# Kernel optimization log

Hardware: AMD Instinct MI355X
Metric: run time of the kernel (lower is better)

Reference implementation:

```python
import jax, jax.numpy as jnp
import numpy as np

NUM_HEADS = 16
EMBED_DIM = 1024
HEAD_DIM = EMBED_DIM // NUM_HEADS
REG_LEN = 2048
SUM_LEN = 64
BSZ = 2
REL_DIM = 64
NUM_REL_EMB = 64
MAX_SUMMARY = 64
SCALE = HEAD_DIM ** -0.5


def _ln(x, g, b, eps=1e-5):
    m = jnp.mean(x, axis=-1, keepdims=True)
    v = jnp.mean((x - m) ** 2, axis=-1, keepdims=True)
    return (x - m) * jax.lax.rsqrt(v + eps) * g + b


def setup_inputs() -> dict:
    key = jax.random.key(0)
    ks = jax.random.split(key, 16)
    inp = {}
    inp['reg_x'] = jax.random.normal(ks[0], (REG_LEN, BSZ, EMBED_DIM), jnp.float32)
    inp['sum_token_ids'] = jax.random.randint(ks[1], (BSZ, SUM_LEN), 0, MAX_SUMMARY + 1)
    inp['rel_idx'] = jax.random.randint(ks[2], (BSZ, SUM_LEN + REG_LEN, REG_LEN), 0, NUM_REL_EMB)
    inp['sum_len'] = SUM_LEN
    inp['reg_len'] = REG_LEN
    emb = jax.random.normal(ks[3], (MAX_SUMMARY + 1, EMBED_DIM), jnp.float32) * 0.02
    inp['emb_sum'] = emb.at[0].set(0.0)  # padding_idx = 0
    inp['rel_emb0'] = jax.random.normal(ks[4], (NUM_REL_EMB, REL_DIM), jnp.float32) * 0.02

    def lin(k, din, dout):
        return jax.random.normal(k, (din, dout), jnp.float32) * (1.0 / np.sqrt(din))

    inp['Wq'] = lin(ks[5], EMBED_DIM, EMBED_DIM); inp['bq'] = jnp.zeros((EMBED_DIM,), jnp.float32)
    inp['Wk'] = lin(ks[6], EMBED_DIM, EMBED_DIM); inp['bk'] = jnp.zeros((EMBED_DIM,), jnp.float32)
    inp['Wv'] = lin(ks[7], EMBED_DIM, EMBED_DIM); inp['bv'] = jnp.zeros((EMBED_DIM,), jnp.float32)
    inp['Wr0'] = lin(ks[8], REL_DIM, EMBED_DIM); inp['br0'] = jnp.zeros((EMBED_DIM,), jnp.float32)
    inp['Wk2'] = lin(ks[9], HEAD_DIM, HEAD_DIM); inp['bk2'] = jnp.zeros((HEAD_DIM,), jnp.float32)
    inp['Wv2'] = lin(ks[10], HEAD_DIM, HEAD_DIM); inp['bv2'] = jnp.zeros((HEAD_DIM,), jnp.float32)
    inp['Wo'] = lin(ks[11], EMBED_DIM, EMBED_DIM); inp['bo'] = jnp.zeros((EMBED_DIM,), jnp.float32)
    for name in ['ln_k', 'ln_v', 'ln_k2', 'ln_v2']:
        inp[name + '_g'] = jnp.ones((HEAD_DIM,), jnp.float32)
        inp[name + '_b'] = jnp.zeros((HEAD_DIM,), jnp.float32)
    return inp


def reference(reg_x, sum_token_ids, rel_idx, sum_len, reg_len, emb_sum, rel_emb0,
              Wq, bq, Wk, bk, Wv, bv, Wr0, br0, Wk2, bk2, Wv2, bv2, Wo, bo,
              ln_k_g, ln_k_b, ln_v_g, ln_v_b, ln_k2_g, ln_k2_b, ln_v2_g, ln_v2_b):
    R, B, E = reg_x.shape  # reg_len, bsz, embed_dim
    H, D = NUM_HEADS, HEAD_DIM
    S = sum_token_ids.shape[1]

    # regular K/V projections + per-head LayerNorm
    reg_k = _ln((reg_x @ Wk + bk).reshape(R, B, H, D), ln_k_g, ln_k_b)
    reg_v = _ln((reg_x @ Wv + bv).reshape(R, B, H, D), ln_v_g, ln_v_b)

    # relation-type embedding projection -> [Rrel, H, D]
    r0 = (rel_emb0 @ Wr0 + br0).reshape(NUM_REL_EMB, H, D)

    # --- stage 1: summary tokens attend over regular tokens ---
    sum_x = emb_sum[sum_token_ids.T]                     # [S, B, E]
    sum_q = sum_x.reshape(S, B, H, D) * SCALE
    scores_sum = jnp.einsum('sbhd,kbhd->bhsk', sum_q, reg_k)   # [B,H,S,R]
    qr_sum = jnp.einsum('sbhd,Zhd->bhsZ', sum_q, r0)           # [B,H,S,Rrel]
    idx_sum = rel_idx[:, :S]                                   # [B,S,R]
    scores_sum = scores_sum + jnp.take_along_axis(qr_sum, idx_sum[:, None, :, :], axis=-1)
    w_sum = jax.nn.softmax(scores_sum, axis=-1)
    sum_x2 = jnp.einsum('bhsk,kbhd->sbhd', w_sum, reg_v)       # [S,B,H,D]

    sum_k2 = _ln(sum_x2 @ Wk2 + bk2, ln_k2_g, ln_k2_b)
    sum_v2 = _ln(sum_x2 @ Wv2 + bv2, ln_v2_g, ln_v2_b)

    # --- stage 2: regular tokens attend over [summary ; regular] keys ---
    reg_q = (reg_x @ Wq + bq).reshape(R, B, H, D) * SCALE
    scores_rs = jnp.einsum('qbhd,sbhd->bhqs', reg_q, sum_k2)   # [B,H,R,S]
    scores_rr = jnp.einsum('qbhd,kbhd->bhqk', reg_q, reg_k)    # [B,H,R,R]
    qr_reg = jnp.einsum('qbhd,Zhd->bhqZ', reg_q, r0)
    idx_reg = rel_idx[:, S:]                                   # [B,R,R]
    scores_rr = scores_rr + jnp.take_along_axis(qr_reg, idx_reg[:, None, :, :], axis=-1)
    scores = jnp.concatenate([scores_rs, scores_rr], axis=-1)  # [B,H,R,S+R]
    w = jax.nn.softmax(scores, axis=-1)
    v_all = jnp.concatenate([sum_v2, reg_v], axis=0)           # [S+R,B,H,D]
    attn_out = jnp.einsum('bhqk,kbhd->qbhd', w, v_all).reshape(R, B, E)
    reg_x2 = attn_out @ Wo + bo
    return reg_x2
```

## Files before the change

### kernel.cpp

```cpp
#include <hip/hip_runtime.h>
#include <cstdint>
#include <cstddef>

#define NH   16
#define HD   64
#define RLEN 2048
#define BSZ  2
#define SLEN 64
#define NZ   64
#define ED   1024
#define KTOT 2112
#define NSPLIT 16

#define QSCALE 0.18033688011112042f

typedef __bf16 bf16_t;
typedef bf16_t bf16x8 __attribute__((ext_vector_type(8)));
typedef bf16_t bf16x4 __attribute__((ext_vector_type(4)));
typedef float  f32x4  __attribute__((ext_vector_type(4)));

__device__ __forceinline__ f32x4 mfma16(bf16x8 a, bf16x8 b, f32x4 c) {
    return __builtin_amdgcn_mfma_f32_16x16x32_bf16(a, b, c, 0, 0, 0);
}

__device__ __forceinline__ void dma16(const void* g, void* l) {
    __builtin_amdgcn_global_load_lds(
        (const __attribute__((address_space(1))) unsigned int*)g,
        (__attribute__((address_space(3))) unsigned int*)l, 16, 0, 0);
}


template<int BM>
__global__ __launch_bounds__(256) void gemm_fast(
    const bf16_t* __restrict__ A, const bf16_t* __restrict__ Bt,
    const float* __restrict__ b0, const float* __restrict__ b1,
    const float* __restrict__ b2,
    const float* __restrict__ gk_, const float* __restrict__ bk_,
    const float* __restrict__ gv_, const float* __restrict__ bv_,
    bf16_t* __restrict__ oq, float* __restrict__ o1,
    bf16_t* __restrict__ okf, bf16_t* __restrict__ ovf,
    int M, int K, int N, int mode)
{
    constexpr int MT = BM / 64;
    __shared__ __align__(16) bf16_t As[BM * 64];
    __shared__ __align__(16) bf16_t Bs[128 * 64];
    __shared__ __align__(16) bf16_t trs[64][66];

    const int t = threadIdx.x;
    const int wave = t >> 6, lane = t & 63;
    const int quad = lane >> 4, l15 = lane & 15;
    const int rsub = lane >> 3, gq = lane & 7;
    const int m0 = blockIdx.y * BM, n0 = blockIdx.x * 128;

    f32x4 acc[MT][8];
#pragma unroll
    for (int i = 0; i < MT; i++)
#pragma unroll
        for (int j = 0; j < 8; j++) acc[i][j] = (f32x4){0.f, 0.f, 0.f, 0.f};

    for (int k0 = 0; k0 < K; k0 += 64) {
#pragma unroll
        for (int j = 0; j < BM / 32; j++) {
            int row = wave * (BM / 4) + j * 8 + rsub;
            const bf16_t* g = A + (size_t)(m0 + row) * K + k0 + ((gq ^ (row & 7)) * 8);
            dma16(g, As + (wave * (BM / 4) + j * 8) * 64);
        }
#pragma unroll
        for (int j = 0; j < 4; j++) {
            int row = wave * 32 + j * 8 + rsub;
            const bf16_t* g = Bt + (size_t)(n0 + row) * K + k0 + ((gq ^ (row & 7)) * 8);
            dma16(g, Bs + (wave * 32 + j * 8) * 64);
        }
        __syncthreads();

#pragma unroll
        for (int kk = 0; kk < 2; kk++) {
            const int pg = ((kk * 4 + quad) ^ (l15 & 7)) * 8;
            bf16x8 af[MT], bf[8];
#pragma unroll
            for (int mt = 0; mt < MT; mt++)
                af[mt] = *(const bf16x8*)(As + (wave * (BM / 4) + mt * 16 + l15) * 64 + pg);
#pragma unroll
            for (int nt = 0; nt < 8; nt++)
                bf[nt] = *(const bf16x8*)(Bs + (nt * 16 + l15) * 64 + pg);
#pragma unroll
            for (int mt = 0; mt < MT; mt++)
#pragma unroll
                for (int nt = 0; nt < 8; nt++)
                    acc[mt][nt] = mfma16(af[mt], bf[nt], acc[mt][nt]);
        }
        __syncthreads();
    }

    if (mode == 0) {
#pragma unroll
        for (int mt = 0; mt < MT; mt++)
#pragma unroll
            for (int nt = 0; nt < 8; nt++)
#pragma unroll
                for (int reg = 0; reg < 4; reg++) {
                    int m = m0 + wave * (BM / 4) + mt * 16 + quad * 4 + reg;
                    int n = n0 + nt * 16 + l15;
                    o1[(size_t)m * N + n] = acc[mt][nt][reg] + b0[n];
                }
        return;
    }

    const int seg = n0 >> 10;
    if (seg == 0) {
#pragma unroll
        for (int mt = 0; mt < MT; mt++)
#pragma unroll
            for (int nt = 0; nt < 8; nt++)
#pragma unroll
                for (int reg = 0; reg < 4; reg++) {
                    int m = m0 + wave * (BM / 4) + mt * 16 + quad * 4 + reg;
                    int n = n0 + nt * 16 + l15;
                    float c = acc[mt][nt][reg] + b0[n];
                    int h = n >> 6, d = n & 63;
                    int r = m >> 1, bb2 = m & 1;
                    size_t off = (((size_t)bb2 * NH + h) * RLEN + r) * HD + d;
                    oq[off] = (bf16_t)(c * QSCALE);
                }
        return;
    }

    const int nl0 = n0 & 1023, h0 = nl0 >> 6;
    const float* bias = (seg == 1) ? b1 : b2;
    const float* lg = (seg == 1) ? gk_ : gv_;
    const float* lb = (seg == 1) ? bk_ : bv_;
    float gj[4], bj[4], bsv[2][4];
#pragma unroll
    for (int j = 0; j < 4; j++) { gj[j] = lg[j * 16 + l15]; bj[j] = lb[j * 16 + l15]; }
#pragma unroll
    for (int h2 = 0; h2 < 2; h2++)
#pragma unroll
        for (int j = 0; j < 4; j++)
            bsv[h2][j] = bias[nl0 + (h2 * 4 + j) * 16 + l15];

    if (seg == 1) {
#pragma unroll
        for (int mt = 0; mt < MT; mt++)
#pragma unroll
            for (int reg = 0; reg < 4; reg++) {
                int m = m0 + wave * (BM / 4) + mt * 16 + quad * 4 + reg;
                int r = m >> 1, bb2 = m & 1, rt = r & 63;
#pragma unroll
                for (int h2 = 0; h2 < 2; h2++) {
                    float c[4], s1 = 0.f, s2 = 0.f;
#pragma unroll
                    for (int j = 0; j < 4; j++) {
                        c[j] = acc[mt][h2 * 4 + j][reg] + bsv[h2][j];
                        s1 += c[j]; s2 += c[j] * c[j];
                    }
#pragma unroll
                    for (int o = 1; o < 16; o <<= 1) {
                        s1 += __shfl_xor(s1, o);
                        s2 += __shfl_xor(s2, o);
                    }
                    float mean = s1 * (1.f / 64.f);
                    float rsi = rsqrtf(s2 * (1.f / 64.f) - mean * mean + 1e-5f);
                    size_t base = (size_t)(bb2 * NH + h0 + h2) * 131072
                                + (size_t)(r >> 6) * 4096;
#pragma unroll
                    for (int j = 0; j < 4; j++) {
                        int d = j * 16 + l15;
                        float y = (c[j] - mean) * rsi * gj[j] + bj[j];
                        okf[base + (size_t)((((rt & 3) * 2 + (d >> 5)) * 64
                              + ((d >> 3) & 3) * 16 + (rt >> 2)) * 8 + (d & 7))] = (bf16_t)y;
                    }
                }
            }
    } else {
        const int tidx = m0 >> 7;
        const int dd = t >> 2, rs2 = (t & 3) * 16;
#pragma unroll
        for (int pb = 0; pb < 2; pb++)
#pragma unroll
            for (int h2 = 0; h2 < 2; h2++) {
#pragma unroll
                for (int mt = 0; mt < MT; mt++)
#pragma unroll
                    for (int rsel = 0; rsel < 2; rsel++) {
                        const int reg = pb + 2 * rsel;
                        const int key = wave * (BM / 8) + mt * 8 + quad * 2 + rsel;
                        float c[4], s1 = 0.f, s2 = 0.f;
#pragma unroll
                        for (int j = 0; j < 4; j++) {
                            c[j] = acc[mt][h2 * 4 + j][reg] + bsv[h2][j];
                            s1 += c[j]; s2 += c[j] * c[j];
                        }
#pragma unroll
                        for (int o = 1; o < 16; o <<= 1) {
                            s1 += __shfl_xor(s1, o);
                            s2 += __shfl_xor(s2, o);
                        }
                        float mean = s1 * (1.f / 64.f);
                        float rsi = rsqrtf(s2 * (1.f / 64.f) - mean * mean + 1e-5f);
#pragma unroll
                        for (int j = 0; j < 4; j++) {
                            float y = (c[j] - mean) * rsi * gj[j] + bj[j];
                            trs[key][j * 16 + l15] = (bf16_t)y;
                        }
                    }
                __syncthreads();
                {
                    bf16x8 o0v, o1v;
#pragma unroll
                    for (int j = 0; j < 8; j++) {
                        o0v[j] = trs[rs2 + j][dd];
                        o1v[j] = trs[rs2 + 8 + j][dd];
                    }
                    size_t base = (size_t)(pb * NH + h0 + h2) * 131072;
                    size_t off0 = base + (size_t)((((tidx * 4 + (dd >> 4)) * 2 + (rs2 >> 5)) * 64
                                  + ((rs2 >> 3) & 3) * 16 + (dd & 15)) * 8);
                    int rsb = rs2 + 8;
                    size_t off1 = base + (size_t)((((tidx * 4 + (dd >> 4)) * 2 + (rsb >> 5)) * 64
                                  + ((rsb >> 3) & 3) * 16 + (dd & 15)) * 8);
                    *(bf16x8*)(ovf + off0) = o0v;
                    *(bf16x8*)(ovf + off1) = o1v;
                }
                __syncthreads();
            }
    }
}

__global__ __launch_bounds__(256) void prep_batch(
    const float* __restrict__ regx, bf16_t* __restrict__ xb,
    const float* __restrict__ Wq, const float* __restrict__ Wk,
    const float* __restrict__ Wv, const float* __restrict__ Wo,
    bf16_t* __restrict__ wqt, bf16_t* __restrict__ wkt,
    bf16_t* __restrict__ wvt, bf16_t* __restrict__ wot,
    const float* __restrict__ emb, const int* __restrict__ ids,
    bf16_t* __restrict__ sum_q,
    const float* __restrict__ rel_emb0, const float* __restrict__ Wr0,
    const float* __restrict__ br0, float* __restrict__ r0out)
{
    const int t = threadIdx.x;
    if (blockIdx.x < 4096) {
        int i = (blockIdx.x * 256 + t) * 4;
        float4 v = *(const float4*)(regx + i);
        bf16x4 o;
        o[0] = (bf16_t)v.x; o[1] = (bf16_t)v.y; o[2] = (bf16_t)v.z; o[3] = (bf16_t)v.w;
        *(bf16x4*)(xb + i) = o;
        return;
    }
    const int bid = blockIdx.x - 4096;

    if (bid >= 1152) {
        const int h = bid - 1152;
        __shared__ float relT[64][65];
        __shared__ float Wl[64][64];
#pragma unroll
        for (int i = 0; i < 4; i++) {
            int idx = t + i * 256;
            int rr = idx >> 4, c4 = (idx & 15) * 4;
            float4 rv = *(const float4*)(rel_emb0 + rr * 64 + c4);
            relT[c4][rr] = rv.x; relT[c4 + 1][rr] = rv.y;
            relT[c4 + 2][rr] = rv.z; relT[c4 + 3][rr] = rv.w;
            float4 wv = *(const float4*)(Wr0 + (size_t)rr * ED + h * 64 + c4);
            *(float4*)(&Wl[rr][c4]) = wv;
        }
        __syncthreads();
        const int z = t & 63, dq = t >> 6;
        float a2[16];
#pragma unroll
        for (int i = 0; i < 16; i++) a2[i] = br0[h * 64 + dq * 16 + i];
        for (int k = 0; k < 64; k++) {
            float r = relT[k][z];
#pragma unroll
            for (int i = 0; i < 16; i++) a2[i] += r * Wl[k][dq * 16 + i];
        }
        float* dst = r0out + ((size_t)h * NZ + z) * HD + dq * 16;
#pragma unroll
        for (int i = 0; i < 4; i++)
            *(float4*)(dst + i * 4) = *(float4*)(&a2[i * 4]);
        return;
    }
    if (bid >= 1024) {
        int sb = bid - 1024;
        int s = sb >> 1, b = sb & 1;
        int id = ids[b * SLEN + s];
        const float* src = emb + (size_t)id * ED;
        for (int e = t; e < ED; e += 256) {
            int h = e >> 6, d = e & 63;
            sum_q[(((size_t)b * NH + h) * SLEN + s) * HD + d] = (bf16_t)(src[e] * QSCALE);
        }
        return;
    }

    __shared__ float tile[64][65];
    int sel = bid >> 8, local = bid & 255;
    const float* src = (sel == 0) ? Wq : (sel == 1) ? Wk : (sel == 2) ? Wv : Wo;
    bf16_t* dst = (sel == 0) ? wqt : (sel == 1) ? wkt : (sel == 2) ? wvt : wot;
    const int R = ED, C = ED;
    const int r0 = (local >> 4) * 64, c0 = (local & 15) * 64;
#pragma unroll
    for (int i = 0; i < 4; i++) {
        int idx = t + i * 256;
        int r = idx >> 4, c = (idx & 15) * 4;
        float4 vv = *(const float4*)(src + (size_t)(r0 + r) * C + c0 + c);
        tile[r][c] = vv.x; tile[r][c + 1] = vv.y; tile[r][c + 2] = vv.z; tile[r][c + 3] = vv.w;
    }
    __syncthreads();
    int cc = t >> 2, rs = (t & 3) * 16;
    bf16x8 o0, o1;
#pragma unroll
    for (int j = 0; j < 8; j++) {
        o0[j] = (bf16_t)tile[rs + j][cc];
        o1[j] = (bf16_t)tile[rs + 8 + j][cc];
    }
    *(bf16x8*)(dst + (size_t)(c0 + cc) * R + r0 + rs) = o0;
    *(bf16x8*)(dst + (size_t)(c0 + cc) * R + r0 + rs + 8) = o1;
}

template<int MT>
__device__ __forceinline__ void attn_tile(
    const bf16_t* __restrict__ ktn, const bf16_t* __restrict__ vtn, int koffn,
    const int* __restrict__ relbase, bool userel,
    const float* __restrict__ qrsw, bf16_t* __restrict__ Psw,
    const bf16x8 (&qf)[MT][2],
    bf16x8 (&kf)[4][2], bf16x8 (&vf)[4][2], int4 (&crel)[MT][4],
    f32x4 (&O)[MT][4], float (&l_i)[MT][4],
    int quad, int l15, int lane)
{
    f32x4 S[MT][4];
    __builtin_amdgcn_s_setprio(1);
#pragma unroll
    for (int mt = 0; mt < MT; mt++)
#pragma unroll
        for (int nt = 0; nt < 4; nt++) {
            f32x4 acc = (f32x4){0.f, 0.f, 0.f, 0.f};
            acc = mfma16(qf[mt][0], kf[nt][0], acc);
            acc = mfma16(qf[mt][1], kf[nt][1], acc);
            S[mt][nt] = acc;
        }
    __builtin_amdgcn_s_setprio(0);

#pragma unroll
    for (int nt = 0; nt < 4; nt++)
#pragma unroll
        for (int kb = 0; kb < 2; kb++)
            kf[nt][kb] = *(const bf16x8*)(ktn + ((nt * 2 + kb) * 64 + lane) * 8);

    if (userel) {
#pragma unroll
        for (int mt = 0; mt < MT; mt++)
#pragma unroll
            for (int reg = 0; reg < 4; reg++) {
                const float* qr = qrsw + (mt * 16 + quad * 4 + reg) * 64;
                int4 c = crel[mt][reg];
                S[mt][0][reg] += qr[c.x];
                S[mt][1][reg] += qr[c.y];
                S[mt][2][reg] += qr[c.z];
                S[mt][3][reg] += qr[c.w];
            }
    }

#pragma unroll
    for (int mt = 0; mt < MT; mt++)
#pragma unroll
        for (int reg = 0; reg < 4; reg++)
            crel[mt][reg] = *(const int4*)(relbase + (size_t)(mt * 16 + reg) * RLEN + koffn);

#pragma unroll
    for (int mt = 0; mt < MT; mt++)
#pragma unroll
        for (int nt = 0; nt < 4; nt++)
#pragma unroll
            for (int reg = 0; reg < 4; reg++)
                S[mt][nt][reg] = exp2f(S[mt][nt][reg]);

    bf16x8 ones;
#pragma unroll
    for (int j = 0; j < 8; j++) ones[j] = (bf16_t)1.0f;

#pragma unroll
    for (int mt = 0; mt < MT; mt++)
#pragma unroll
        for (int reg = 0; reg < 4; reg++) {
            bf16x4 pv;
            pv[0] = (bf16_t)S[mt][0][reg]; pv[1] = (bf16_t)S[mt][1][reg];
            pv[2] = (bf16_t)S[mt][2][reg]; pv[3] = (bf16_t)S[mt][3][reg];
            *(bf16x4*)(Psw + (mt * 16 + quad * 4 + reg) * 72 + 4 * l15) = pv;
        }

    __builtin_amdgcn_s_setprio(1);
#pragma unroll
    for (int mt = 0; mt < MT; mt++) {
        bf16x8 pf0 = *(const bf16x8*)(Psw + (mt * 16 + l15) * 72 + quad * 8);
        bf16x8 pf1 = *(const bf16x8*)(Psw + (mt * 16 + l15) * 72 + 32 + quad * 8);
        f32x4 ls = (f32x4){0.f, 0.f, 0.f, 0.f};
        ls = mfma16(pf0, ones, ls);
        ls = mfma16(pf1, ones, ls);
#pragma unroll
        for (int nt = 0; nt < 4; nt++) {
            O[mt][nt] = mfma16(pf0, vf[nt][0], O[mt][nt]);
            O[mt][nt] = mfma16(pf1, vf[nt][1], O[mt][nt]);
        }
#pragma unroll
        for (int reg = 0; reg < 4; reg++) l_i[mt][reg] += ls[reg];
    }
    __builtin_amdgcn_s_setprio(0);

#pragma unroll
    for (int nt = 0; nt < 4; nt++)
#pragma unroll
        for (int kb = 0; kb < 2; kb++)
            vf[nt][kb] = *(const bf16x8*)(vtn + ((nt * 2 + kb) * 64 + lane) * 8);
}

__device__ __forceinline__ void load_kv(
    bf16x8 (&kf)[4][2], bf16x8 (&vf)[4][2],
    const bf16_t* __restrict__ kt, const bf16_t* __restrict__ vt, int lane)
{
#pragma unroll
    for (int nt = 0; nt < 4; nt++)
#pragma unroll
        for (int kb = 0; kb < 2; kb++) {
            kf[nt][kb] = *(const bf16x8*)(kt + ((nt * 2 + kb) * 64 + lane) * 8);
            vf[nt][kb] = *(const bf16x8*)(vt + ((nt * 2 + kb) * 64 + lane) * 8);
        }
}

template<int MT>
__device__ __forceinline__ void build_qr(
    const float* __restrict__ r0, int h, const bf16x8 (&qf)[MT][2],
    float* __restrict__ qrsw, int quad, int l15)
{
#pragma unroll
    for (int nt = 0; nt < 4; nt++) {
        const float* rp = r0 + ((size_t)h * NZ + l15 + 16 * nt) * HD + quad * 8;
        float4 a0 = *(const float4*)(rp);
        float4 a1 = *(const float4*)(rp + 4);
        bf16x8 bf0;
        bf0[0] = (bf16_t)a0.x; bf0[1] = (bf16_t)a0.y; bf0[2] = (bf16_t)a0.z; bf0[3] = (bf16_t)a0.w;
        bf0[4] = (bf16_t)a1.x; bf0[5] = (bf16_t)a1.y; bf0[6] = (bf16_t)a1.z; bf0[7] = (bf16_t)a1.w;
        float4 b0 = *(const float4*)(rp + 32);
        float4 b1 = *(const float4*)(rp + 36);
        bf16x8 bf1;
        bf1[0] = (bf16_t)b0.x; bf1[1] = (bf16_t)b0.y; bf1[2] = (bf16_t)b0.z; bf1[3] = (bf16_t)b0.w;
        bf1[4] = (bf16_t)b1.x; bf1[5] = (bf16_t)b1.y; bf1[6] = (bf16_t)b1.z; bf1[7] = (bf16_t)b1.w;
#pragma unroll
        for (int mt = 0; mt < MT; mt++) {
            f32x4 qa = (f32x4){0.f, 0.f, 0.f, 0.f};
            qa = mfma16(qf[mt][0], bf0, qa);
            qa = mfma16(qf[mt][1], bf1, qa);
#pragma unroll
            for (int reg = 0; reg < 4; reg++)
                qrsw[(mt * 16 + quad * 4 + reg) * 64 + l15 + 16 * nt] = qa[reg];
        }
    }
}

__global__ __launch_bounds__(256) void sum_attn_split(
    const bf16_t* __restrict__ Qb,
    const bf16_t* __restrict__ kfm, const bf16_t* __restrict__ vfm,
    const float*  __restrict__ r0,
    const int*    __restrict__ rel_idx,
    float* __restrict__ po, float* __restrict__ pl)
{
    constexpr int TPS = 32 / NSPLIT;
    const int bh = blockIdx.x;
    const int split = blockIdx.y;
    const int b = bh >> 4, h = bh & 15;
    const int t = threadIdx.x;
    const int wave = t >> 6, lane = t & 63;
    const int quad = lane >> 4, l15 = lane & 15;

    __shared__ __align__(16) bf16_t Ps[4][16 * 72];
    __shared__ float qrs[4][16 * 64];

    bf16x8 qf[1][2];
    const bf16_t* Qrow = Qb + ((size_t)bh * SLEN + wave * 16 + l15) * HD;
    qf[0][0] = *(const bf16x8*)(Qrow + quad * 8);
    qf[0][1] = *(const bf16x8*)(Qrow + 32 + quad * 8);

    const int* relbase = rel_idx + ((size_t)b * KTOT + wave * 16 + quad * 4) * RLEN + 4 * l15;
    const bf16_t* kbase = kfm + (size_t)bh * 131072 + (size_t)(split * TPS) * 4096;
    const bf16_t* vbase = vfm + (size_t)bh * 131072 + (size_t)(split * TPS) * 4096;

    bf16x8 kf[4][2], vf[4][2];
    int4 crel[1][4];
    load_kv(kf, vf, kbase, vbase, lane);
#pragma unroll
    for (int reg = 0; reg < 4; reg++)
        crel[0][reg] = *(const int4*)(relbase + (size_t)reg * RLEN + split * TPS * 64);

    build_qr<1>(r0, h, qf, qrs[wave], quad, l15);

    f32x4 O[1][4];
    float l_i[1][4];
#pragma unroll
    for (int nt = 0; nt < 4; nt++) O[0][nt] = (f32x4){0.f, 0.f, 0.f, 0.f};
#pragma unroll
    for (int r = 0; r < 4; r++) l_i[0][r] = 0.f;

    for (int i = 0; i < TPS; i++) {
        const int nx = (i < TPS - 1) ? i + 1 : i;
        attn_tile<1>(kbase + (size_t)nx * 4096, vbase + (size_t)nx * 4096,
                     (split * TPS + nx) * 64, relbase, true,
                     qrs[wave], Ps[wave], qf, kf, vf, crel,
                     O, l_i, quad, l15, lane);
    }

    const size_t pslot = (size_t)bh * NSPLIT + split;
#pragma unroll
    for (int nt = 0; nt < 4; nt++)
#pragma unroll
        for (int reg = 0; reg < 4; reg++) {
            int sq = wave * 16 + quad * 4 + reg;
            po[(pslot * SLEN + sq) * HD + l15 + 16 * nt] = O[0][nt][reg];
        }
#pragma unroll
    for (int reg = 0; reg < 4; reg++) {
        int sq = wave * 16 + quad * 4 + reg;
        if (l15 == 0) pl[pslot * SLEN + sq] = l_i[0][reg];
    }
}

__global__ __launch_bounds__(64) void k2v2_fused(
    const float* __restrict__ po, const float* __restrict__ pl,
    const float* __restrict__ Wk2, const float* __restrict__ bk2,
    const float* __restrict__ Wv2, const float* __restrict__ bv2,
    const float* __restrict__ gk, const float* __restrict__ bk,
    const float* __restrict__ gv, const float* __restrict__ bv,
    bf16_t* __restrict__ k2fm, bf16_t* __restrict__ v2fm)
{
    int row = blockIdx.x;
    int d = threadIdx.x;
    int bh = row >> 6, s = row & 63;

    float L = 0.f, acc = 0.f;
#pragma unroll
    for (int j = 0; j < NSPLIT; j++) {
        L += pl[((size_t)bh * NSPLIT + j) * SLEN + s];
        acc += po[(((size_t)bh * NSPLIT + j) * SLEN + s) * HD + d];
    }
    __shared__ float xs[64];
    xs[d] = acc / L;
    __syncthreads();

#pragma unroll
    for (int which = 0; which < 2; which++) {
        const float* W  = which ? Wv2 : Wk2;
        const float* bi = which ? bv2 : bk2;
        const float* g  = which ? gv : gk;
        const float* bb = which ? bv : bk;
        float a = bi[d];
#pragma unroll
        for (int j = 0; j < 64; j++) a += xs[j] * W[j * HD + d];
        float s1 = a, s2 = a * a;
#pragma unroll
        for (int o = 32; o > 0; o >>= 1) {
            s1 += __shfl_xor(s1, o);
            s2 += __shfl_xor(s2, o);
        }
        float mean = s1 * (1.f / 64.f);
        float var  = s2 * (1.f / 64.f) - mean * mean;
        float y = (a - mean) * rsqrtf(var + 1e-5f) * g[d] + bb[d];
        if (which == 0) {
            size_t off = (size_t)bh * 4096 +
                (size_t)((((s & 3) * 2 + (d >> 5)) * 64
                          + ((d >> 3) & 3) * 16 + (s >> 2)) * 8 + (d & 7));
            k2fm[off] = (bf16_t)y;
        } else {
            size_t off = (size_t)bh * 4096 +
                (size_t)((((d >> 4) * 2 + (s >> 5)) * 64
                          + ((s >> 3) & 3) * 16 + (d & 15)) * 8 + (s & 7));
            v2fm[off] = (bf16_t)y;
        }
    }
}

__global__ __launch_bounds__(256) void reg_attn_mfma(
    const bf16_t* __restrict__ Qb,
    const bf16_t* __restrict__ kfm, const bf16_t* __restrict__ vfm,
    const bf16_t* __restrict__ k2fm, const bf16_t* __restrict__ v2fm,
    const float*  __restrict__ r0,
    const int*    __restrict__ rel_idx,
    bf16_t* __restrict__ attn_out)
{
    const int bid = blockIdx.x;
    const int bh = (bid & 7) * 4 + ((bid >> 3) & 3);
    const int qt = bid >> 5;
    const int b = bh >> 4, h = bh & 15;
    const int q0 = qt * 128;

    const int t = threadIdx.x;
    const int wave = t >> 6, lane = t & 63;
    const int quad = lane >> 4, l15 = lane & 15;

    __shared__ __align__(16) bf16_t Ps[4][32 * 72];
    __shared__ float qrs[4][32 * 64];

    bf16x8 qf[2][2];
#pragma unroll
    for (int mt = 0; mt < 2; mt++) {
        const bf16_t* Qrow = Qb + ((size_t)bh * RLEN + q0 + wave * 32 + mt * 16 + l15) * HD;
        qf[mt][0] = *(const bf16x8*)(Qrow + quad * 8);
        qf[mt][1] = *(const bf16x8*)(Qrow + 32 + quad * 8);
    }

    bf16x8 kf[4][2], vf[4][2];
    int4 crel[2][4];
    load_kv(kf, vf, k2fm + (size_t)bh * 4096, v2fm + (size_t)bh * 4096, lane);

    build_qr<2>(r0, h, qf, qrs[wave], quad, l15);

    f32x4 O[2][4];
    float l_i[2][4];
#pragma unroll
    for (int mt = 0; mt < 2; mt++)
#pragma unroll
        for (int nt = 0; nt < 4; nt++) O[mt][nt] = (f32x4){0.f, 0.f, 0.f, 0.f};
#pragma unroll
    for (int mt = 0; mt < 2; mt++)
#pragma unroll
        for (int r = 0; r < 4; r++) l_i[mt][r] = 0.f;

    const int* relbase = rel_idx +
        ((size_t)b * KTOT + SLEN + q0 + wave * 32 + quad * 4) * RLEN + 4 * l15;

    const bf16_t* kt = kfm + (size_t)bh * 131072;
    const bf16_t* vt = vfm + (size_t)bh * 131072;

    attn_tile<2>(kt, vt, 0, relbase, false, qrs[wave], Ps[wave], qf,
                 kf, vf, crel, O, l_i, quad, l15, lane);

    for (int tile = 0; tile < 32; tile++) {
        const int nx = (tile < 31) ? tile + 1 : tile;
        attn_tile<2>(kt + (size_t)nx * 4096, vt + (size_t)nx * 4096, nx * 64,
                     relbase, true, qrs[wave], Ps[wave], qf,
                     kf, vf, crel, O, l_i, quad, l15, lane);
    }

#pragma unroll
    for (int mt = 0; mt < 2; mt++) {
        float linv[4];
#pragma unroll
        for (int reg = 0; reg < 4; reg++) linv[reg] = 1.0f / l_i[mt][reg];
#pragma unroll
        for (int nt = 0; nt < 4; nt++)
#pragma unroll
            for (int reg = 0; reg < 4; reg++) {
                int q = q0 + wave * 32 + mt * 16 + quad * 4 + reg;
                attn_out[((size_t)q * BSZ + b) * ED + h * HD + l15 + 16 * nt] =
                    (bf16_t)(O[mt][nt][reg] * linv[reg]);
            }
    }
}

extern "C" void kernel_launch(void* const* d_in, const int* in_sizes, int n_in,
                              void* d_out, int out_size, void* d_ws, size_t ws_size,
                              hipStream_t stream)
{
    const float* reg_x    = (const float*)d_in[0];
    const int*   sum_ids  = (const int*)d_in[1];
    const int*   rel_idx  = (const int*)d_in[2];
    const float* emb_sum  = (const float*)d_in[5];
    const float* rel_emb0 = (const float*)d_in[6];
    const float* Wq = (const float*)d_in[7];
    const float* bq = (const float*)d_in[8];
    const float* Wk = (const float*)d_in[9];
    const float* bk = (const float*)d_in[10];
    const float* Wv = (const float*)d_in[11];
    const float* bv = (const float*)d_in[12];
    const float* Wr0 = (const float*)d_in[13];
    const float* br0 = (const float*)d_in[14];
    const float* Wk2 = (const float*)d_in[15];
    const float* bk2 = (const float*)d_in[16];
    const float* Wv2 = (const float*)d_in[17];
    const float* bv2 = (const float*)d_in[18];
    const float* Wo  = (const float*)d_in[19];
    const float* bo  = (const float*)d_in[20];
    const float* ln_k_g  = (const float*)d_in[21];
    const float* ln_k_b  = (const float*)d_in[22];
    const float* ln_v_g  = (const float*)d_in[23];
    const float* ln_v_b  = (const float*)d_in[24];
    const float* ln_k2_g = (const float*)d_in[25];
    const float* ln_k2_b = (const float*)d_in[26];
    const float* ln_v2_g = (const float*)d_in[27];
    const float* ln_v2_b = (const float*)d_in[28];

    const size_t QKV = (size_t)BSZ * NH * RLEN * HD;
    const size_t SUM = (size_t)BSZ * NH * SLEN * HD;

    float*  r0   = (float*)d_ws;
    bf16_t* xb   = (bf16_t*)(r0 + (size_t)NH * NZ * HD);
    bf16_t* qb   = xb + QKV;
    bf16_t* kfm  = qb + QKV;
    bf16_t* vfm  = kfm + QKV;
    bf16_t* sqb  = vfm + QKV;
    bf16_t* k2fm = sqb + SUM;
    bf16_t* v2fm = k2fm + SUM;
    bf16_t* wqt  = v2fm + SUM;
    bf16_t* wkt  = wqt + (size_t)ED * ED;
    bf16_t* wvt  = wkt + (size_t)ED * ED;
    bf16_t* wot  = wvt + (size_t)ED * ED;
    float*  po   = (float*)(wot + (size_t)ED * ED);
    float*  pl   = po + (size_t)BSZ * NH * NSPLIT * SLEN * HD;
    bf16_t* aob  = (bf16_t*)po;

    const int M = RLEN * BSZ;

    prep_batch<<<4096 + 1168, 256, 0, stream>>>(
        reg_x, xb, Wq, Wk, Wv, Wo,
        wqt, wkt, wvt, wot,
        emb_sum, sum_ids, sqb, rel_emb0, Wr0, br0, r0);

    gemm_fast<128><<<dim3(3 * ED / 128, M / 128), 256, 0, stream>>>(
        xb, wqt, bq, bk, bv, ln_k_g, ln_k_b, ln_v_g, ln_v_b,
        qb, nullptr, kfm, vfm, M, ED, 3 * ED, 1);

    sum_attn_split<<<dim3(BSZ * NH, NSPLIT), 256, 0, stream>>>(sqb, kfm, vfm, r0, rel_idx, po, pl);

    k2v2_fused<<<BSZ * NH * SLEN, 64, 0, stream>>>(po, pl, Wk2, bk2, Wv2, bv2,
                                                   ln_k2_g, ln_k2_b, ln_v2_g, ln_v2_b,
                                                   k2fm, v2fm);

    reg_attn_mfma<<<512, 256, 0, stream>>>(qb, kfm, vfm, k2fm, v2fm, r0, rel_idx, aob);

    gemm_fast<64><<<dim3(ED / 128, M / 64), 256, 0, stream>>>(
        aob, wot, bo, nullptr, nullptr, nullptr, nullptr, nullptr, nullptr,
        nullptr, (float*)d_out, nullptr, nullptr, M, ED, ED, 0);
}
```

Baseline: 340.1 us.

## Split key range across wave pairs in regular attention and merge via LDS

Each block of the regular-token attention kernel now covers 64 queries instead of 128. Two wave pairs process the first and second halves of the key tiles, and the grid doubles to 1024 blocks. The partial outputs and row sums of the second half are written to shared memory and added into the first half before normalisation. The aim is more parallelism and shorter per-wave serial key loops, at the cost of duplicated Q/qr setup, two extra block barriers and an LDS reduction.

```diff
diff --git a/kernel.cpp b/kernel.cpp
--- a/kernel.cpp
+++ b/kernel.cpp
@@ -583,71 +583,110 @@
 {
     const int bid = blockIdx.x;
     const int bh = (bid & 7) * 4 + ((bid >> 3) & 3);
-    const int qt = bid >> 5;
+    const int rg = bid >> 5;
     const int b = bh >> 4, h = bh & 15;
-    const int q0 = qt * 128;
+    const int q0 = rg * 64;
 
     const int t = threadIdx.x;
     const int wave = t >> 6, lane = t & 63;
+    const int wq2 = wave & 1, half = wave >> 1;
     const int quad = lane >> 4, l15 = lane & 15;
 
     __shared__ __align__(16) bf16_t Ps[4][32 * 72];
-    __shared__ float qrs[4][32 * 64];
+    __shared__ __align__(16) float qrs[2][32 * 64];
+    __shared__ float lsh[2][32];
 
     bf16x8 qf[2][2];
 #pragma unroll
     for (int mt = 0; mt < 2; mt++) {
-        const bf16_t* Qrow = Qb + ((size_t)bh * RLEN + q0 + wave * 32 + mt * 16 + l15) * HD;
+        const bf16_t* Qrow = Qb + ((size_t)bh * RLEN + q0 + wq2 * 32 + mt * 16 + l15) * HD;
         qf[mt][0] = *(const bf16x8*)(Qrow + quad * 8);
         qf[mt][1] = *(const bf16x8*)(Qrow + 32 + quad * 8);
     }
 
+    build_qr<2>(r0, h, qf, qrs[wq2], quad, l15);
+
+    f32x4 O[2][4];
+    float l_i[2][4];
+#pragma unroll
+    for (int mt = 0; mt < 2; mt++)
+#pragma unroll
+        for (int nt = 0; nt < 4; nt++) O[mt][nt] = (f32x4){0.f, 0.f, 0.f, 0.f};
+#pragma unroll
+    for (int mt = 0; mt < 2; mt++)
+#pragma unroll
+        for (int r = 0; r < 4; r++) l_i[mt][r] = 0.f;
+
+    const int* relbase = rel_idx +
+        ((size_t)b * KTOT + SLEN + q0 + wq2 * 32 + quad * 4) * RLEN + 4 * l15;
+
+    const bf16_t* kt = kfm + (size_t)bh * 131072;
+    const bf16_t* vt = vfm + (size_t)bh * 131072;
+
     bf16x8 kf[4][2], vf[4][2];
     int4 crel[2][4];
-    load_kv(kf, vf, k2fm + (size_t)bh * 4096, v2fm + (size_t)bh * 4096, lane);
-
-    build_qr<2>(r0, h, qf, qrs[wave], quad, l15);
-
-    f32x4 O[2][4];
-    float l_i[2][4];
-#pragma unroll
-    for (int mt = 0; mt < 2; mt++)
-#pragma unroll
-        for (int nt = 0; nt < 4; nt++) O[mt][nt] = (f32x4){0.f, 0.f, 0.f, 0.f};
-#pragma unroll
-    for (int mt = 0; mt < 2; mt++)
-#pragma unroll
-        for (int r = 0; r < 4; r++) l_i[mt][r] = 0.f;
-
-    const int* relbase = rel_idx +
-        ((size_t)b * KTOT + SLEN + q0 + wave * 32 + quad * 4) * RLEN + 4 * l15;
-
-    const bf16_t* kt = kfm + (size_t)bh * 131072;
-    const bf16_t* vt = vfm + (size_t)bh * 131072;
-
-    attn_tile<2>(kt, vt, 0, relbase, false, qrs[wave], Ps[wave], qf,
-                 kf, vf, crel, O, l_i, quad, l15, lane);
-
-    for (int tile = 0; tile < 32; tile++) {
-        const int nx = (tile < 31) ? tile + 1 : tile;
-        attn_tile<2>(kt + (size_t)nx * 4096, vt + (size_t)nx * 4096, nx * 64,
-                     relbase, true, qrs[wave], Ps[wave], qf,
+
+    if (half == 0) {
+        load_kv(kf, vf, k2fm + (size_t)bh * 4096, v2fm + (size_t)bh * 4096, lane);
+        attn_tile<2>(kt, vt, 0, relbase, false, qrs[wq2], Ps[wave], qf,
                      kf, vf, crel, O, l_i, quad, l15, lane);
-    }
-
-#pragma unroll
-    for (int mt = 0; mt < 2; mt++) {
-        float linv[4];
-#pragma unroll
-        for (int reg = 0; reg < 4; reg++) linv[reg] = 1.0f / l_i[mt][reg];
-#pragma unroll
-        for (int nt = 0; nt < 4; nt++)
-#pragma unroll
-            for (int reg = 0; reg < 4; reg++) {
-                int q = q0 + wave * 32 + mt * 16 + quad * 4 + reg;
-                attn_out[((size_t)q * BSZ + b) * ED + h * HD + l15 + 16 * nt] =
-                    (bf16_t)(O[mt][nt][reg] * linv[reg]);
-            }
+        for (int tile = 0; tile < 16; tile++) {
+            const int nx = (tile < 15) ? tile + 1 : tile;
+            attn_tile<2>(kt + (size_t)nx * 4096, vt + (size_t)nx * 4096, nx * 64,
+                         relbase, true, qrs[wq2], Ps[wave], qf,
+                         kf, vf, crel, O, l_i, quad, l15, lane);
+        }
+    } else {
+        load_kv(kf, vf, kt + (size_t)16 * 4096, vt + (size_t)16 * 4096, lane);
+#pragma unroll
+        for (int mt = 0; mt < 2; mt++)
+#pragma unroll
+            for (int reg = 0; reg < 4; reg++)
+                crel[mt][reg] = *(const int4*)(relbase + (size_t)(mt * 16 + reg) * RLEN + 16 * 64);
+        for (int tile = 16; tile < 32; tile++) {
+            const int nx = (tile < 31) ? tile + 1 : tile;
+            attn_tile<2>(kt + (size_t)nx * 4096, vt + (size_t)nx * 4096, nx * 64,
+                         relbase, true, qrs[wq2], Ps[wave], qf,
+                         kf, vf, crel, O, l_i, quad, l15, lane);
+        }
+    }
+
+    __syncthreads();
+    if (half == 1) {
+        float* osh = qrs[wq2];
+#pragma unroll
+        for (int mt = 0; mt < 2; mt++) {
+#pragma unroll
+            for (int nt = 0; nt < 4; nt++)
+#pragma unroll
+                for (int reg = 0; reg < 4; reg++)
+                    osh[(mt * 16 + quad * 4 + reg) * 64 + l15 + 16 * nt] = O[mt][nt][reg];
+            if (l15 == 0)
+#pragma unroll
+                for (int reg = 0; reg < 4; reg++)
+                    lsh[wq2][mt * 16 + quad * 4 + reg] = l_i[mt][reg];
+        }
+    }
+    __syncthreads();
+    if (half == 0) {
+        const float* osh = qrs[wq2];
+#pragma unroll
+        for (int mt = 0; mt < 2; mt++) {
+            float linv[4];
+#pragma unroll
+            for (int reg = 0; reg < 4; reg++)
+                linv[reg] = 1.0f / (l_i[mt][reg] + lsh[wq2][mt * 16 + quad * 4 + reg]);
+#pragma unroll
+            for (int nt = 0; nt < 4; nt++)
+#pragma unroll
+                for (int reg = 0; reg < 4; reg++) {
+                    int q = q0 + wq2 * 32 + mt * 16 + quad * 4 + reg;
+                    float ot = O[mt][nt][reg]
+                             + osh[(mt * 16 + quad * 4 + reg) * 64 + l15 + 16 * nt];
+                    attn_out[((size_t)q * BSZ + b) * ED + h * HD + l15 + 16 * nt] =
+                        (bf16_t)(ot * linv[reg]);
+                }
+        }
     }
 }
 
@@ -719,7 +758,7 @@
                                                    ln_k2_g, ln_k2_b, ln_v2_g, ln_v2_b,
                                                    k2fm, v2fm);
 
-    reg_attn_mfma<<<512, 256, 0, stream>>>(qb, kfm, vfm, k2fm, v2fm, r0, rel_idx, aob);
+    reg_attn_mfma<<<1024, 256, 0, stream>>>(qb, kfm, vfm, k2fm, v2fm, r0, rel_idx, aob);
 
     gemm_fast<64><<<dim3(ED / 128, M / 64), 256, 0, stream>>>(
         aob, wot, bo, nullptr, nullptr, nullptr, nullptr, nullptr, nullptr,
```

After: 346.2 us. No clear change (+1.8%).
